# Performance work log

Hardware: AMD Instinct MI355X
Metric: run time of the kernel (lower is better)

## Reference

```python
import jax, jax.numpy as jnp
import numpy as np

HEADS = 16
ROPE_BASE = 10000.0


def rotate_half(x):
    h = x.shape[-1] // 2
    x1, x2 = x[..., :h], x[..., h:]
    return jnp.concatenate((-x2, x1), axis=-1)


def rope_cos_sin(L, head_dim, dtype):
    inv_freq = 1.0 / (ROPE_BASE ** (jnp.arange(0, head_dim, 2, dtype=jnp.float32) / head_dim))
    t = jnp.arange(L, dtype=jnp.float32)
    freqs = jnp.einsum('i,j->ij', t, inv_freq)          # [L, head_dim/2]
    emb = jnp.concatenate((freqs, freqs), axis=-1)      # [L, head_dim]
    return jnp.cos(emb).astype(dtype), jnp.sin(emb).astype(dtype)


def setup_inputs() -> dict:
    key = jax.random.key(0)
    ks = jax.random.split(key, 5)
    B, L, D = 2, 2048, 1024
    s = 0.02
    return {
        'x': jax.random.normal(ks[0], (B, L, D), dtype=jnp.float32),
        'Wqkv': jax.random.normal(ks[1], (D, 3 * D), dtype=jnp.float32) * s,
        'bqkv': jnp.zeros((3 * D,), dtype=jnp.float32),
        'Wout': jax.random.normal(ks[2], (D, D), dtype=jnp.float32) * s,
        'bout': jnp.zeros((D,), dtype=jnp.float32),
    }


def reference(x, Wqkv, bqkv, Wout, bout):
    B, L, D = x.shape
    H = HEADS
    hd = D // H
    scale = hd ** -0.5

    qkv = x @ Wqkv + bqkv                               # [B, L, 3D]
    qkv = qkv.reshape(B, L, 3, H, hd).transpose(2, 0, 3, 1, 4)  # [3, B, H, L, hd]
    q, k, v = qkv[0], qkv[1], qkv[2]

    cos, sin = rope_cos_sin(L, hd, x.dtype)             # [L, hd] each, broadcast over B,H
    q = q * cos + rotate_half(q) * sin
    k = k * cos + rotate_half(k) * sin

    attn = jnp.einsum('bhqd,bhkd->bhqk', q, k) * scale  # [B, H, L, L]
    attn = jax.nn.softmax(attn, axis=-1)
    out = jnp.einsum('bhqk,bhkd->bhqd', attn, v)        # [B, H, L, hd]
    out = out.transpose(0, 2, 1, 3).reshape(B, L, D)
    return out @ Wout + bout
```

## Files before the change

### kernel.cpp

```cpp
#include <hip/hip_runtime.h>
#include <stdint.h>
#include <stddef.h>


typedef short          bf16x8 __attribute__((ext_vector_type(8)));
typedef float          f32x4  __attribute__((ext_vector_type(4)));
typedef unsigned short u16x4  __attribute__((ext_vector_type(4)));
typedef unsigned short u16x8  __attribute__((ext_vector_type(8)));

#define B_   2
#define L_   2048
#define D_   1024
#define H_   16
#define HD_  64
#define BL_  4096
#define LOG2E 1.4426950408889634f
#define QSC  0.18033688011112042f

__device__ __forceinline__ unsigned short f2bf(float f) {
  unsigned int u = __float_as_uint(f);
  u += 0x7FFFu + ((u >> 16) & 1u);
  return (unsigned short)(u >> 16);
}
__device__ __forceinline__ float bf2f(unsigned short h) {
  return __uint_as_float(((unsigned int)h) << 16);
}
__device__ __forceinline__ uint32_t cvtpk_bf16(float lo, float hi) {
  uint32_t r;
  asm("v_cvt_pk_bf16_f32 %0, %1, %2" : "=v"(r) : "v"(lo), "v"(hi));
  return r;
}
__device__ __forceinline__ float fast_exp2(float x) {
  float r;
  asm("v_exp_f32 %0, %1" : "=v"(r) : "v"(x));
  return r;
}

__device__ __forceinline__ void gload_lds16(const unsigned short* g, unsigned short* l) {
  __builtin_amdgcn_global_load_lds(
      (__attribute__((address_space(1))) void*)g,
      (__attribute__((address_space(3))) void*)l, 16, 0, 0);
}

__device__ __forceinline__ void transpose_tile(
    const float* __restrict__ src, unsigned short* __restrict__ dst,
    int K, int N, int n0, int k0, int tid, float (*tile)[33]) {
  const int tx = tid & 31, ty = tid >> 5;
#pragma unroll
  for (int i = 0; i < 4; ++i)
    tile[ty * 4 + i][tx] = src[(size_t)(k0 + ty * 4 + i) * N + n0 + tx];
  __syncthreads();
#pragma unroll
  for (int i = 0; i < 4; ++i)
    dst[(size_t)(n0 + ty * 4 + i) * K + k0 + tx] = f2bf(tile[tx][ty * 4 + i]);
}

__global__ void __launch_bounds__(256)
prep_kernel(const float* __restrict__ x,
            const float* __restrict__ Wqkv,
            const float* __restrict__ Wout,
            u16x8* __restrict__ xb,
            unsigned short* __restrict__ WqkvT,
            unsigned short* __restrict__ WoutT,
            float2* __restrict__ rtbl) {
  __shared__ float tile[32][33];
  const int bid = blockIdx.x, tid = threadIdx.x;
  if (bid < 2048) {
    const int i = bid * 256 + tid;
    const float4 a = ((const float4*)x)[2 * i];
    const float4 b = ((const float4*)x)[2 * i + 1];
    u16x8 o;
    o[0] = f2bf(a.x); o[1] = f2bf(a.y); o[2] = f2bf(a.z); o[3] = f2bf(a.w);
    o[4] = f2bf(b.x); o[5] = f2bf(b.y); o[6] = f2bf(b.z); o[7] = f2bf(b.w);
    xb[i] = o;
  } else if (bid < 2304) {
    const int i = (bid - 2048) * 256 + tid;
    const int pos = i >> 5, j = i & 31;
    const float inv = exp2f(-(float)j * 0.4152410118609203f);
    float s, c;
    sincosf((float)pos * inv, &s, &c);
    rtbl[i] = make_float2(c, s);
  } else if (bid < 5376) {
    const int t = bid - 2304;
    transpose_tile(Wqkv, WqkvT, D_, 3 * D_, (t % 96) * 32, (t / 96) * 32, tid, tile);
  } else {
    const int t = bid - 5376;
    transpose_tile(Wout, WoutT, D_, D_, (t % 32) * 32, (t / 32) * 32, tid, tile);
  }
}

__global__ void __launch_bounds__(512)
gemm1_256(const unsigned short* __restrict__ A,
          const unsigned short* __restrict__ Bt,
          const float* __restrict__ bias,
          const float2* __restrict__ rt,
          unsigned short* __restrict__ Qb,
          unsigned short* __restrict__ Kb,
          unsigned short* __restrict__ Vt) {
  __shared__ unsigned short As[2][16384];
  __shared__ unsigned short Bs[2][16384];
  const int tid = threadIdx.x;
  const int w = tid >> 6, l = tid & 63;
  const int lg = l >> 4, ll = l & 15;
  const int wr = w >> 2, wc = w & 3;
  const int lid = (blockIdx.x & 7) * 24 + (blockIdx.x >> 3);
  const int n0 = (lid % 12) * 256, m0 = (lid / 12) * 256;

  f32x4 acc[8][4] = {};

  int srcOff[4];
#pragma unroll
  for (int c = 0; c < 4; ++c) {
    const int idx = c * 512 + tid;
    const int row = idx >> 3, slot = idx & 7;
    srcOff[c] = row * 1024 + ((slot ^ (row & 7)) << 3);
  }
  const unsigned short* gA = A + (size_t)m0 * 1024;
  const unsigned short* gB = Bt + (size_t)n0 * 1024;

  auto stageAll = [&](int bsel, int kt) {
    const int kk = kt * 64;
#pragma unroll
    for (int c = 0; c < 4; ++c)
      gload_lds16(gA + srcOff[c] + kk, &As[bsel][c * 4096 + w * 512]);
#pragma unroll
    for (int c = 0; c < 4; ++c)
      gload_lds16(gB + srcOff[c] + kk, &Bs[bsel][c * 4096 + w * 512]);
  };

  auto rdA = [&](const unsigned short* base, int mi, int kk) -> bf16x8 {
    const int row = wr * 128 + mi * 16 + ll;
    return *(const bf16x8*)((const char*)base + row * 128 +
                            ((kk * 64 + lg * 16) ^ ((ll & 7) << 4)));
  };
  auto rdB = [&](const unsigned short* base, int ni, int kk) -> bf16x8 {
    const int row = wc * 64 + ni * 16 + ll;
    return *(const bf16x8*)((const char*)base + row * 128 +
                            ((kk * 64 + lg * 16) ^ ((ll & 7) << 4)));
  };

  auto ktile = [&](const unsigned short* pa, const unsigned short* pb,
                   int nxtb, int nxtkt) {
    bf16x8 bfr[4], afr[4];
#pragma unroll
    for (int ni = 0; ni < 4; ++ni) bfr[ni] = rdB(pb, ni, 0);
#pragma unroll
    for (int mi = 0; mi < 4; ++mi) afr[mi] = rdA(pa, mi, 0);
    if (nxtkt < 16) stageAll(nxtb, nxtkt);
    __builtin_amdgcn_s_barrier();
    asm volatile("s_waitcnt lgkmcnt(0)" ::: "memory");
    __builtin_amdgcn_sched_barrier(0);
    __builtin_amdgcn_s_setprio(1);
#pragma unroll
    for (int mi = 0; mi < 4; ++mi)
#pragma unroll
      for (int ni = 0; ni < 4; ++ni)
        acc[mi][ni] = __builtin_amdgcn_mfma_f32_16x16x32_bf16(afr[mi], bfr[ni], acc[mi][ni], 0, 0, 0);
    __builtin_amdgcn_s_setprio(0);
    __builtin_amdgcn_s_barrier();
#pragma unroll
    for (int mi = 0; mi < 4; ++mi) afr[mi] = rdA(pa, 4 + mi, 0);
    __builtin_amdgcn_s_barrier();
    asm volatile("s_waitcnt lgkmcnt(0)" ::: "memory");
    __builtin_amdgcn_sched_barrier(0);
    __builtin_amdgcn_s_setprio(1);
#pragma unroll
    for (int mi = 0; mi < 4; ++mi)
#pragma unroll
      for (int ni = 0; ni < 4; ++ni)
        acc[4 + mi][ni] = __builtin_amdgcn_mfma_f32_16x16x32_bf16(afr[mi], bfr[ni], acc[4 + mi][ni], 0, 0, 0);
    __builtin_amdgcn_s_setprio(0);
    __builtin_amdgcn_s_barrier();
#pragma unroll
    for (int ni = 0; ni < 4; ++ni) bfr[ni] = rdB(pb, ni, 1);
#pragma unroll
    for (int mi = 0; mi < 4; ++mi) afr[mi] = rdA(pa, mi, 1);
    __builtin_amdgcn_s_barrier();
    asm volatile("s_waitcnt lgkmcnt(0)" ::: "memory");
    __builtin_amdgcn_sched_barrier(0);
    __builtin_amdgcn_s_setprio(1);
#pragma unroll
    for (int mi = 0; mi < 4; ++mi)
#pragma unroll
      for (int ni = 0; ni < 4; ++ni)
        acc[mi][ni] = __builtin_amdgcn_mfma_f32_16x16x32_bf16(afr[mi], bfr[ni], acc[mi][ni], 0, 0, 0);
    __builtin_amdgcn_s_setprio(0);
    __builtin_amdgcn_s_barrier();
#pragma unroll
    for (int mi = 0; mi < 4; ++mi) afr[mi] = rdA(pa, 4 + mi, 1);
    __builtin_amdgcn_s_barrier();
    asm volatile("s_waitcnt lgkmcnt(0)" ::: "memory");
    __builtin_amdgcn_sched_barrier(0);
    __builtin_amdgcn_s_setprio(1);
#pragma unroll
    for (int mi = 0; mi < 4; ++mi)
#pragma unroll
      for (int ni = 0; ni < 4; ++ni)
        acc[4 + mi][ni] = __builtin_amdgcn_mfma_f32_16x16x32_bf16(afr[mi], bfr[ni], acc[4 + mi][ni], 0, 0, 0);
    __builtin_amdgcn_s_setprio(0);
    asm volatile("s_waitcnt vmcnt(0)" ::: "memory");
    __builtin_amdgcn_s_barrier();
  };

  stageAll(0, 0);
  asm volatile("s_waitcnt vmcnt(0)" ::: "memory");
  __syncthreads();
#pragma unroll 1
  for (int it = 0; it < 8; ++it) {
    ktile(&As[0][0], &Bs[0][0], 1, 2 * it + 1);
    ktile(&As[1][0], &Bs[1][0], 0, 2 * it + 2);
  }

  const int t = (n0 + wc * 64) >> 10;
  if (t == 2) {
#pragma unroll
    for (int ni = 0; ni < 4; ++ni) {
      const int n = n0 + wc * 64 + ni * 16 + ll;
      const float bv = bias[n];
      const int r = n & 1023;
      const int h = r >> 6, d = r & 63;
#pragma unroll
      for (int mi = 0; mi < 8; ++mi) {
        const int row0 = m0 + wr * 128 + mi * 16 + lg * 4;
        const int b   = row0 >> 11;
        const int pos = row0 & 2047;
        const int bh  = b * H_ + h;
        const int wb  = (pos >> 2) & 7;
        const int posS = (pos & ~31) + 8 * (wb & 3) + 4 * (wb >> 2);
        u16x4 pk;
#pragma unroll
        for (int rg = 0; rg < 4; ++rg) pk[rg] = f2bf(acc[mi][ni][rg] + bv);
        *(u16x4*)(Vt + ((size_t)bh * HD_ + d) * L_ + posS) = pk;
      }
    }
  } else {
    unsigned short* dst = (t == 0) ? Qb : Kb;
    const float qsc = (t == 0) ? QSC : 1.0f;
    const int h = ((n0 + wc * 64) & 1023) >> 6;
#pragma unroll
    for (int ni = 0; ni < 2; ++ni) {
      const int d = ni * 16 + ll;
      const float bv1 = bias[n0 + wc * 64 + ni * 16 + ll];
      const float bv2 = bias[n0 + wc * 64 + (ni + 2) * 16 + ll];
#pragma unroll
      for (int mi = 0; mi < 8; ++mi) {
        const int row0 = m0 + wr * 128 + mi * 16 + lg * 4;
        const int b   = row0 >> 11;
        const int pos0 = row0 & 2047;
        unsigned short* base = dst + (size_t)(b * H_ + h) * L_ * HD_;
#pragma unroll
        for (int rg = 0; rg < 4; ++rg) {
          const int pos = pos0 + rg;
          const float2 cs = rt[pos * 32 + d];
          const float q1 = acc[mi][ni][rg] + bv1;
          const float q2 = acc[mi][ni + 2][rg] + bv2;
          base[(size_t)pos * HD_ + d]      = f2bf((q1 * cs.x - q2 * cs.y) * qsc);
          base[(size_t)pos * HD_ + d + 32] = f2bf((q2 * cs.x + q1 * cs.y) * qsc);
        }
      }
    }
  }
}

__global__ void __launch_bounds__(256)
gemm_bt1(const unsigned short* __restrict__ A,
         const unsigned short* __restrict__ Bt,
         const float* __restrict__ bias,
         float* __restrict__ outF,
         int M, int N, int K) {
  __shared__ unsigned short As[2][128 * 32];
  __shared__ unsigned short Bs[2][128 * 32];
  const int tid = threadIdx.x;
  const int w = tid >> 6, l = tid & 63;
  const int lg = l >> 4, ll = l & 15;
  const int cpx = gridDim.x >> 3;
  const int lid = (blockIdx.x & 7) * cpx + (blockIdx.x >> 3);
  const int nx = N >> 7;
  const int n0 = (lid % nx) * 128, m0 = (lid / nx) * 128;
  const int wm = (w >> 1) * 64, wn = (w & 1) * 64;

  f32x4 acc[4][4] = {};

  const int srow = w * 16 + (l >> 2);
  const int scol = (l & 3) * 8;
  const unsigned short* gA = A  + (size_t)(m0 + srow) * K + scol;
  const unsigned short* gB = Bt + (size_t)(n0 + srow) * K + scol;
  const int ldsoff = (w * 1024) >> 1;

  const int NT = K >> 5;
  int buf = 0;

  auto stage = [&](int bsel, int kt) {
    const int kk = kt * 32;
#pragma unroll
    for (int c = 0; c < 2; ++c) {
      gload_lds16(gA + (size_t)c * 64 * K + kk, &As[bsel][ldsoff + c * 2048]);
      gload_lds16(gB + (size_t)c * 64 * K + kk, &Bs[bsel][ldsoff + c * 2048]);
    }
  };

  stage(0, 0);
  for (int kt = 0; kt < NT; ++kt) {
    __syncthreads();
    if (kt + 1 < NT) stage(buf ^ 1, kt + 1);
    const unsigned short* pa = &As[buf][0];
    const unsigned short* pb = &Bs[buf][0];
    bf16x8 af[4], bfv[4];
#pragma unroll
    for (int mi = 0; mi < 4; ++mi)
      af[mi] = *(const bf16x8*)(pa + (wm + mi * 16 + ll) * 32 + 8 * lg);
#pragma unroll
    for (int ni = 0; ni < 4; ++ni)
      bfv[ni] = *(const bf16x8*)(pb + (wn + ni * 16 + ll) * 32 + 8 * lg);
    __builtin_amdgcn_s_setprio(1);
#pragma unroll
    for (int mi = 0; mi < 4; ++mi)
#pragma unroll
      for (int ni = 0; ni < 4; ++ni)
        acc[mi][ni] = __builtin_amdgcn_mfma_f32_16x16x32_bf16(
            af[mi], bfv[ni], acc[mi][ni], 0, 0, 0);
    __builtin_amdgcn_s_setprio(0);
    buf ^= 1;
  }

#pragma unroll
  for (int ni = 0; ni < 4; ++ni) {
    const int n = n0 + wn + ni * 16 + ll;
    const float bv = bias[n];
#pragma unroll
    for (int mi = 0; mi < 4; ++mi) {
      const int row0 = m0 + wm + mi * 16 + lg * 4;
#pragma unroll
      for (int rg = 0; rg < 4; ++rg)
        outF[(size_t)(row0 + rg) * N + n] = acc[mi][ni][rg] + bv;
    }
  }
}

__global__ void __launch_bounds__(512)
attn_kernel(const unsigned short* __restrict__ Qb,
            const unsigned short* __restrict__ Kb,
            const unsigned short* __restrict__ Vt,
            unsigned short* __restrict__ Ob) {
  __shared__ unsigned short Ks[2][2][4096];
  __shared__ unsigned short Vs[2][2][4096];
  const int tid = threadIdx.x, w = tid >> 6, l = tid & 63;
  const int lg = l >> 4, ll = l & 15;
  const int bid = ((blockIdx.x & 7) << 6) + (blockIdx.x >> 3);
  const int bh  = bid >> 4;
  const int q0  = (bid & 15) * 128;
  const unsigned short* Qp = Qb + ((size_t)bh * L_ + q0 + w * 16) * HD_;
  const unsigned short* Kp = Kb + (size_t)bh * L_ * HD_;
  const unsigned short* Vp = Vt + (size_t)bh * HD_ * L_;

  const int srow = tid >> 3;
  const int scol = ((tid & 7) ^ (srow & 7)) * 8;
  auto stage = [&](int bsel, int kv0) {
#pragma unroll
    for (int c = 0; c < 2; ++c) {
      gload_lds16(Kp + (size_t)(kv0 + c * 64 + srow) * HD_ + scol, &Ks[bsel][c][w * 512]);
      gload_lds16(Vp + (size_t)srow * L_ + kv0 + c * 64 + scol, &Vs[bsel][c][w * 512]);
    }
  };

  bf16x8 qf[2];
#pragma unroll
  for (int ks = 0; ks < 2; ++ks)
    qf[ks] = *(const bf16x8*)(Qp + (size_t)ll * HD_ + ks * 32 + 8 * lg);

  bf16x8 ones;
#pragma unroll
  for (int j = 0; j < 8; ++j) ones[j] = (short)0x3F80;

  f32x4 o[4] = {};
  f32x4 osum = {};

  stage(0, 0);
  __syncthreads();

  int buf = 0;
  for (int t = 0; t < 16; ++t) {
    if (t + 1 < 16) stage(buf ^ 1, (t + 1) * 128);
    f32x4 s[2][4];

#pragma unroll
    for (int kc = 0; kc < 2; ++kc) {
      const char* Ksb = (const char*)&Ks[buf][kc][0];
      bf16x8 kfr[4][2];
#pragma unroll
      for (int ni = 0; ni < 4; ++ni)
#pragma unroll
        for (int ks = 0; ks < 2; ++ks)
          kfr[ni][ks] = *(const bf16x8*)(Ksb + (ni * 16 + ll) * 128 +
                                         ((ks * 64 + lg * 16) ^ ((ll & 7) << 4)));
#pragma unroll
      for (int ni = 0; ni < 4; ++ni) s[kc][ni] = f32x4{0.f, 0.f, 0.f, 0.f};
      __builtin_amdgcn_s_setprio(1);
#pragma unroll
      for (int ks = 0; ks < 2; ++ks)
#pragma unroll
        for (int ni = 0; ni < 4; ++ni)
          s[kc][ni] = __builtin_amdgcn_mfma_f32_16x16x32_bf16(kfr[ni][ks], qf[ks], s[kc][ni], 0, 0, 0);
      __builtin_amdgcn_s_setprio(0);
    }

    bf16x8 pa[2][2];
#pragma unroll
    for (int kc = 0; kc < 2; ++kc) {
      uint32_t wd[4][2];
#pragma unroll
      for (int ni = 0; ni < 4; ++ni) {
        const float p0 = fast_exp2(s[kc][ni][0]);
        const float p1 = fast_exp2(s[kc][ni][1]);
        const float p2 = fast_exp2(s[kc][ni][2]);
        const float p3 = fast_exp2(s[kc][ni][3]);
        wd[ni][0] = cvtpk_bf16(p0, p1);
        wd[ni][1] = cvtpk_bf16(p2, p3);
      }
#pragma unroll
      for (int ks = 0; ks < 2; ++ks) {
        union { uint32_t u[4]; bf16x8 v; } pu;
        pu.u[0] = wd[2 * ks][0];     pu.u[1] = wd[2 * ks][1];
        pu.u[2] = wd[2 * ks + 1][0]; pu.u[3] = wd[2 * ks + 1][1];
        pa[kc][ks] = pu.v;
      }
    }

#pragma unroll
    for (int kc = 0; kc < 2; ++kc) {
      const char* Vsb = (const char*)&Vs[buf][kc][0];
      bf16x8 vf[2][4];
#pragma unroll
      for (int ks = 0; ks < 2; ++ks)
#pragma unroll
        for (int ni = 0; ni < 4; ++ni)
          vf[ks][ni] = *(const bf16x8*)(Vsb + (ni * 16 + ll) * 128 +
                                        ((ks * 64 + lg * 16) ^ ((ll & 7) << 4)));
      __builtin_amdgcn_s_setprio(1);
#pragma unroll
      for (int ks = 0; ks < 2; ++ks) {
#pragma unroll
        for (int ni = 0; ni < 4; ++ni)
          o[ni] = __builtin_amdgcn_mfma_f32_16x16x32_bf16(pa[kc][ks], vf[ks][ni], o[ni], 0, 0, 0);
        osum = __builtin_amdgcn_mfma_f32_16x16x32_bf16(pa[kc][ks], ones, osum, 0, 0, 0);
      }
      __builtin_amdgcn_s_setprio(0);
    }

    __syncthreads();
    buf ^= 1;
  }

  const int b = bh >> 4, h = bh & 15;
  unsigned short* Op = Ob + ((size_t)b * L_ + q0 + w * 16) * D_ + h * HD_;
#pragma unroll
  for (int rg = 0; rg < 4; ++rg) {
    const float iq = 1.0f / osum[rg];
#pragma unroll
    for (int ni = 0; ni < 4; ++ni)
      Op[(size_t)(lg * 4 + rg) * D_ + ni * 16 + ll] = f2bf(o[ni][rg] * iq);
  }
}

extern "C" void kernel_launch(void* const* d_in, const int* in_sizes, int n_in,
                              void* d_out, int out_size, void* d_ws, size_t ws_size,
                              hipStream_t stream) {
  const float* x    = (const float*)d_in[0];
  const float* Wqkv = (const float*)d_in[1];
  const float* bqkv = (const float*)d_in[2];
  const float* Wout = (const float*)d_in[3];
  const float* bout = (const float*)d_in[4];
  float* out = (float*)d_out;

  char* ws = (char*)d_ws;
  unsigned short* xb    = (unsigned short*)(ws);
  unsigned short* WqkvT = (unsigned short*)(ws + (8ull  << 20));
  unsigned short* WoutT = (unsigned short*)(ws + (14ull << 20));
  unsigned short* Qb    = (unsigned short*)(ws + (16ull << 20));
  unsigned short* Kb    = (unsigned short*)(ws + (24ull << 20));
  unsigned short* Vt    = (unsigned short*)(ws + (32ull << 20));
  unsigned short* Ob    = (unsigned short*)(ws + (40ull << 20));
  float2* rtbl = (float2*)(ws + (40ull << 20));

  prep_kernel<<<6400, 256, 0, stream>>>(x, Wqkv, Wout, (u16x8*)xb, WqkvT, WoutT, rtbl);

  gemm1_256<<<192, 512, 0, stream>>>(xb, WqkvT, bqkv, rtbl, Qb, Kb, Vt);

  attn_kernel<<<B_ * H_ * (L_ / 128), 512, 0, stream>>>(Qb, Kb, Vt, Ob);

  gemm_bt1<<<(D_ / 128) * (BL_ / 128), 256, 0, stream>>>(
      Ob, WoutT, bout, out, BL_, D_, D_);
}
```

Baseline: 113.5 us.

## Split global-to-LDS staging into two phases and deepen QKV GEMM prefetch

Restructures the QKV projection GEMM main loop so that each k-tile's global-to-LDS loads are split into two stages (B plus half of A, then the other half of A). These stages are issued at different points between MFMA quads, and both buffers are prefilled before the loop. Partial vmcnt waits replace the full drain at the end of every k-tile, and the per-quad lgkmcnt waits and sched barriers are removed. The goal is to keep more global loads in flight while MFMAs run and to cut barrier stalls. The risk is that the buffer-reuse ordering and the vmcnt counts must be exactly right to avoid races.

Result: no change. 112.7 us (-0.7%).

```diff
diff --git a/kernel.cpp b/kernel.cpp
--- a/kernel.cpp
+++ b/kernel.cpp
@@ -118,14 +118,20 @@
   const unsigned short* gA = A + (size_t)m0 * 1024;
   const unsigned short* gB = Bt + (size_t)n0 * 1024;
 
-  auto stageAll = [&](int bsel, int kt) {
+  auto stageS1 = [&](int kt) {
+    const int bsel = kt & 1;
     const int kk = kt * 64;
-#pragma unroll
-    for (int c = 0; c < 4; ++c)
-      gload_lds16(gA + srcOff[c] + kk, &As[bsel][c * 4096 + w * 512]);
 #pragma unroll
     for (int c = 0; c < 4; ++c)
       gload_lds16(gB + srcOff[c] + kk, &Bs[bsel][c * 4096 + w * 512]);
+    gload_lds16(gA + srcOff[0] + kk, &As[bsel][0 * 4096 + w * 512]);
+    gload_lds16(gA + srcOff[2] + kk, &As[bsel][2 * 4096 + w * 512]);
+  };
+  auto stageS2 = [&](int kt) {
+    const int bsel = kt & 1;
+    const int kk = kt * 64;
+    gload_lds16(gA + srcOff[1] + kk, &As[bsel][1 * 4096 + w * 512]);
+    gload_lds16(gA + srcOff[3] + kk, &As[bsel][3 * 4096 + w * 512]);
   };
 
   auto rdA = [&](const unsigned short* base, int mi, int kk) -> bf16x8 {
@@ -139,17 +145,14 @@
                             ((kk * 64 + lg * 16) ^ ((ll & 7) << 4)));
   };
 
-  auto ktile = [&](const unsigned short* pa, const unsigned short* pb,
-                   int nxtb, int nxtkt) {
-    bf16x8 bfr[4], afr[4];
-#pragma unroll
-    for (int ni = 0; ni < 4; ++ni) bfr[ni] = rdB(pb, ni, 0);
-#pragma unroll
-    for (int mi = 0; mi < 4; ++mi) afr[mi] = rdA(pa, mi, 0);
-    if (nxtkt < 16) stageAll(nxtb, nxtkt);
-    __builtin_amdgcn_s_barrier();
-    asm volatile("s_waitcnt lgkmcnt(0)" ::: "memory");
-    __builtin_amdgcn_sched_barrier(0);
+  auto quadA = [&](int bsel, int kk, bf16x8 (&bfr)[4]) {
+    const unsigned short* pb = &Bs[bsel][0];
+    const unsigned short* pa = &As[bsel][0];
+#pragma unroll
+    for (int ni = 0; ni < 4; ++ni) bfr[ni] = rdB(pb, ni, kk);
+    bf16x8 afr[4];
+#pragma unroll
+    for (int mi = 0; mi < 4; ++mi) afr[mi] = rdA(pa, mi, kk);
     __builtin_amdgcn_s_setprio(1);
 #pragma unroll
     for (int mi = 0; mi < 4; ++mi)
@@ -157,12 +160,12 @@
       for (int ni = 0; ni < 4; ++ni)
         acc[mi][ni] = __builtin_amdgcn_mfma_f32_16x16x32_bf16(afr[mi], bfr[ni], acc[mi][ni], 0, 0, 0);
     __builtin_amdgcn_s_setprio(0);
-    __builtin_amdgcn_s_barrier();
-#pragma unroll
-    for (int mi = 0; mi < 4; ++mi) afr[mi] = rdA(pa, 4 + mi, 0);
-    __builtin_amdgcn_s_barrier();
-    asm volatile("s_waitcnt lgkmcnt(0)" ::: "memory");
-    __builtin_amdgcn_sched_barrier(0);
+  };
+  auto quadB = [&](int bsel, int kk, bf16x8 (&bfr)[4]) {
+    const unsigned short* pa = &As[bsel][0];
+    bf16x8 afr[4];
+#pragma unroll
+    for (int mi = 0; mi < 4; ++mi) afr[mi] = rdA(pa, 4 + mi, kk);
     __builtin_amdgcn_s_setprio(1);
 #pragma unroll
     for (int mi = 0; mi < 4; ++mi)
@@ -170,45 +173,35 @@
       for (int ni = 0; ni < 4; ++ni)
         acc[4 + mi][ni] = __builtin_amdgcn_mfma_f32_16x16x32_bf16(afr[mi], bfr[ni], acc[4 + mi][ni], 0, 0, 0);
     __builtin_amdgcn_s_setprio(0);
+  };
+
+  stageS1(0); stageS2(0); stageS1(1); stageS2(1);
+  asm volatile("s_waitcnt vmcnt(0)" ::: "memory");
+  __builtin_amdgcn_s_barrier();
+
+#pragma unroll 1
+  for (int t = 0; t < 8; ++t) {
+    bf16x8 bfr[4];
+    const int ba = (2 * t) & 1;
+    if (t >= 1) stageS2(2 * t + 1);
+    quadA(ba, 0, bfr);
+    quadB(ba, 0, bfr);
+    quadA(ba, 1, bfr);
     __builtin_amdgcn_s_barrier();
-#pragma unroll
-    for (int ni = 0; ni < 4; ++ni) bfr[ni] = rdB(pb, ni, 1);
-#pragma unroll
-    for (int mi = 0; mi < 4; ++mi) afr[mi] = rdA(pa, mi, 1);
+    if (2 * t + 2 < 16) stageS1(2 * t + 2);
+    quadB(ba, 1, bfr);
+    if (t == 7) { asm volatile("s_waitcnt vmcnt(0)" ::: "memory"); }
+    else        { asm volatile("s_waitcnt vmcnt(6)" ::: "memory"); }
     __builtin_amdgcn_s_barrier();
-    asm volatile("s_waitcnt lgkmcnt(0)" ::: "memory");
-    __builtin_amdgcn_sched_barrier(0);
-    __builtin_amdgcn_s_setprio(1);
-#pragma unroll
-    for (int mi = 0; mi < 4; ++mi)
-#pragma unroll
-      for (int ni = 0; ni < 4; ++ni)
-        acc[mi][ni] = __builtin_amdgcn_mfma_f32_16x16x32_bf16(afr[mi], bfr[ni], acc[mi][ni], 0, 0, 0);
-    __builtin_amdgcn_s_setprio(0);
+    if (2 * t + 2 < 16) stageS2(2 * t + 2);
+    quadA(ba ^ 1, 0, bfr);
+    quadB(ba ^ 1, 0, bfr);
+    quadA(ba ^ 1, 1, bfr);
     __builtin_amdgcn_s_barrier();
-#pragma unroll
-    for (int mi = 0; mi < 4; ++mi) afr[mi] = rdA(pa, 4 + mi, 1);
+    if (2 * t + 3 < 16) stageS1(2 * t + 3);
+    quadB(ba ^ 1, 1, bfr);
+    asm volatile("s_waitcnt vmcnt(6)" ::: "memory");
     __builtin_amdgcn_s_barrier();
-    asm volatile("s_waitcnt lgkmcnt(0)" ::: "memory");
-    __builtin_amdgcn_sched_barrier(0);
-    __builtin_amdgcn_s_setprio(1);
-#pragma unroll
-    for (int mi = 0; mi < 4; ++mi)
-#pragma unroll
-      for (int ni = 0; ni < 4; ++ni)
-        acc[4 + mi][ni] = __builtin_amdgcn_mfma_f32_16x16x32_bf16(afr[mi], bfr[ni], acc[4 + mi][ni], 0, 0, 0);
-    __builtin_amdgcn_s_setprio(0);
-    asm volatile("s_waitcnt vmcnt(0)" ::: "memory");
-    __builtin_amdgcn_s_barrier();
-  };
-
-  stageAll(0, 0);
-  asm volatile("s_waitcnt vmcnt(0)" ::: "memory");
-  __syncthreads();
-#pragma unroll 1
-  for (int it = 0; it < 8; ++it) {
-    ktile(&As[0][0], &Bs[0][0], 1, 2 * it + 1);
-    ktile(&As[1][0], &Bs[1][0], 0, 2 * it + 2);
   }
 
   const int t = (n0 + wc * 64) >> 10;
```
